# Optimization experiments

Measured on AMD Instinct MI355X. Metric: run time of the kernel, lower is better.

The kernel has to match this reference:

```python
import jax, jax.numpy as jnp
import numpy as np

B, IN, OUT = 8192, 4096, 2048  # OUT must equal 32*64 per betta/gamma sizes


def setup_inputs() -> dict:
    key = jax.random.key(0)
    kx, kw = jax.random.split(key, 2)
    X = jax.random.normal(kx, (B, IN), dtype=jnp.float32)
    # xavier-uniform-like init for W
    limit = float(np.sqrt(6.0 / (IN + OUT)))
    W = jax.random.uniform(kw, (IN, OUT), minval=-limit, maxval=limit, dtype=jnp.float32)
    absmean = jnp.abs(W).mean(axis=0)
    alpha = jnp.abs(W).mean()          # scalar, >= 0
    betta = absmean[:32]               # (32,), >= 0
    gamma = absmean[32:96]             # (64,), >= 0
    return {"X": X, "W": W, "alpha": alpha, "betta": betta, "gamma": gamma}


def reference(X, W, alpha, betta, gamma):
    # module applies relu_ to alpha/betta/gamma data before the functional call
    alpha = jax.nn.relu(alpha)
    betta = jax.nn.relu(betta)
    gamma = jax.nn.relu(gamma)
    X_bin = jnp.sign(X)                # (B, IN)
    W_bin = jnp.sign(W)                # (IN, OUT)
    # scale[i*64+j] = alpha * betta[i] * gamma[j] -> (OUT,)
    scale = (alpha * jnp.outer(betta, gamma)).reshape(-1)
    return (X_bin @ W_bin) * scale     # (B, OUT)
```

## Files before the change

### kernel.cpp

```cpp
#include <hip/hip_runtime.h>


#define M_DIM 8192
#define K_DIM 4096
#define N_DIM 2048
#define NTK   (K_DIM / 128)
#define PANEL (128 * 128 * 16)
#define KTILE 8192

typedef int i32x4 __attribute__((ext_vector_type(4)));
typedef int i32x8 __attribute__((ext_vector_type(8)));
typedef float f32x16 __attribute__((ext_vector_type(16)));

__device__ __forceinline__ unsigned int nib4(float x) {
  unsigned int s = (__float_as_uint(x) >> 28) & 0x8u;
  return x == 0.0f ? 0u : (0x2u | s);
}

__device__ __forceinline__ unsigned int pack8(const float* f) {
  unsigned int p = 0;
#pragma unroll
  for (int j = 0; j < 8; ++j) p |= nib4(f[j]) << (4 * j);
  return p;
}

__device__ __forceinline__ void gload_lds16(const void* g, void* lds) {
  __builtin_amdgcn_global_load_lds(
      (const __attribute__((address_space(1))) unsigned int*)g,
      (__attribute__((address_space(3))) unsigned int*)lds, 16, 0, 0);
}

__global__ __launch_bounds__(256) void binX_kernel(
    const float* __restrict__ X, unsigned char* __restrict__ Xq) {
  __shared__ float tile[32][260];
  const int t = threadIdx.x;
  const int rg = blockIdx.x >> 4;
  const int kc = blockIdx.x & 15;
  const int lrow = t >> 6;
  const int col4 = (t & 63) * 4;
#pragma unroll
  for (int i = 0; i < 8; ++i)
    *(float4*)&tile[i * 4 + lrow][col4] =
        *(const float4*)&X[(size_t)(rg * 32 + i * 4 + lrow) * K_DIM + kc * 256 + col4];
  __syncthreads();
  const int s = t >> 5;
  const int r = t & 31;
  float f[32];
#pragma unroll
  for (int q = 0; q < 8; ++q)
    *(float4*)&f[q * 4] = *(const float4*)&tile[r][s * 32 + q * 4];
  uint4 gq;
  gq.x = pack8(f + 0);  gq.y = pack8(f + 8);
  gq.z = pack8(f + 16); gq.w = pack8(f + 24);
  const int row = rg * 32 + r;
  const int kslot = kc * 8 + s;
  unsigned char* dst = Xq + (size_t)(row >> 7) * PANEL +
                       ((size_t)kslot * 128 + (row & 127)) * 16;
  *(uint4*)dst = gq;
}

__global__ __launch_bounds__(256) void binW_kernel(
    const float* __restrict__ W, unsigned char* __restrict__ Wq) {
  __shared__ float tile[32][260];
  const int t = threadIdx.x;
  const int q = blockIdx.x >> 7;
  const int kt = (blockIdx.x >> 3) & 15;
  const int s = blockIdx.x & 7;
#pragma unroll
  for (int i = 0; i < 8; ++i) {
    int row = i * 4 + (t >> 6);
    int col4 = (t & 63) * 4;
    *(float4*)&tile[row][col4] =
        *(const float4*)&W[(size_t)(kt * 256 + s * 32 + row) * N_DIM + q * 256 + col4];
  }
  __syncthreads();
  float f[32];
#pragma unroll
  for (int k = 0; k < 32; ++k) f[k] = tile[k][t];
  uint4 gq;
  gq.x = pack8(f + 0);  gq.y = pack8(f + 8);
  gq.z = pack8(f + 16); gq.w = pack8(f + 24);
  const int n = q * 256 + t;
  const int kslot = kt * 8 + s;
  unsigned char* dst = Wq + (size_t)(n >> 7) * PANEL +
                       ((size_t)kslot * 128 + (n & 127)) * 16;
  *(uint4*)dst = gq;
}

__device__ __forceinline__ void stage_tiles(const unsigned char* __restrict__ Asrc,
                                            const unsigned char* __restrict__ Bsrc,
                                            unsigned char* lds, int t) {
#pragma unroll
  for (int p = 0; p < 2; ++p) {
    int c = p * 256 + t;
    gload_lds16(Asrc + c * 16, lds + c * 16);
    gload_lds16(Bsrc + c * 16, lds + 8192 + c * 16);
  }
}

__global__ __launch_bounds__(256, 4) void gemm_fp4_kernel(
    const unsigned char* __restrict__ Aq,
    const unsigned char* __restrict__ Bq,
    const float* __restrict__ alpha,
    const float* __restrict__ betta,
    const float* __restrict__ gamma,
    float* __restrict__ C) {
  __shared__ __align__(16) unsigned char smem[32768];

  const int t = threadIdx.x;
  const int lane = t & 63;
  const int l31 = lane & 31;
  const int lhi = lane >> 5;
  const int w = t >> 6;
  const int wr = w >> 1;
  const int wc = w & 1;

  const int bid = blockIdx.x;
  const int j = bid >> 3;
  const int bn = j & 15;
  const int bm = (bid & 7) * 8 + (j >> 4);
  const int row0 = bm * 128;
  const int col0 = bn * 128;

  const unsigned char* Abase = Aq + (size_t)bm * PANEL;
  const unsigned char* Bbase = Bq + (size_t)bn * PANEL;

  f32x16 acc[2][2];
#pragma unroll
  for (int fm = 0; fm < 2; ++fm)
#pragma unroll
    for (int fn = 0; fn < 2; ++fn)
#pragma unroll
      for (int r = 0; r < 16; ++r) acc[fm][fn][r] = 0.f;

  i32x8 a8[2], b8[2];
#pragma unroll
  for (int i = 0; i < 2; ++i)
#pragma unroll
    for (int e = 0; e < 8; ++e) { a8[i][e] = 0; b8[i][e] = 0; }

  stage_tiles(Abase, Bbase, &smem[0], t);
  asm volatile("s_waitcnt vmcnt(0)" ::: "memory");
  __builtin_amdgcn_s_barrier();

  for (int kt = 0; kt < NTK; ++kt) {
    const int cur = kt & 1;
    const unsigned char* pA = &smem[cur * 16384];
    const unsigned char* pB = pA + 8192;

    if (kt + 1 < NTK)
      stage_tiles(Abase + (kt + 1) * KTILE, Bbase + (kt + 1) * KTILE,
                  &smem[(cur ^ 1) * 16384], t);

#pragma unroll
    for (int kk = 0; kk < 2; ++kk) {
      const int g = kk * 2 + lhi;
#pragma unroll
      for (int fm = 0; fm < 2; ++fm)
        *(i32x4*)&a8[fm] = *(const i32x4*)&pA[(g * 128 + wr * 64 + fm * 32 + l31) * 16];
#pragma unroll
      for (int fn = 0; fn < 2; ++fn)
        *(i32x4*)&b8[fn] = *(const i32x4*)&pB[(g * 128 + wc * 64 + fn * 32 + l31) * 16];
#pragma unroll
      for (int fm = 0; fm < 2; ++fm)
#pragma unroll
        for (int fn = 0; fn < 2; ++fn)
          acc[fm][fn] = __builtin_amdgcn_mfma_scale_f32_32x32x64_f8f6f4(
              a8[fm], b8[fn], acc[fm][fn], 4, 4,
              0, 0x7F7F7F7F, 0, 0x7F7F7F7F);
    }

    asm volatile("s_waitcnt vmcnt(0)" ::: "memory");
    __builtin_amdgcn_s_barrier();
  }

  const float ra = fmaxf(alpha[0], 0.0f);
#pragma unroll
  for (int fn = 0; fn < 2; ++fn) {
    const int col = col0 + wc * 64 + fn * 32 + l31;
    const float sc = ra * fmaxf(betta[col >> 6], 0.0f) * fmaxf(gamma[col & 63], 0.0f);
#pragma unroll
    for (int fm = 0; fm < 2; ++fm) {
      const int rbase = row0 + wr * 64 + fm * 32 + 4 * lhi;
#pragma unroll
      for (int r = 0; r < 16; ++r) {
        const int row = rbase + (r & 3) + 8 * (r >> 2);
        C[(size_t)row * N_DIM + col] = acc[fm][fn][r] * sc;
      }
    }
  }
}

extern "C" void kernel_launch(void* const* d_in, const int* in_sizes, int n_in,
                              void* d_out, int out_size, void* d_ws, size_t ws_size,
                              hipStream_t stream) {
  const float* X = (const float*)d_in[0];
  const float* W = (const float*)d_in[1];
  const float* alpha = (const float*)d_in[2];
  const float* betta = (const float*)d_in[3];
  const float* gamma = (const float*)d_in[4];
  float* out = (float*)d_out;

  unsigned char* Xq = (unsigned char*)d_ws;
  unsigned char* Wq = Xq + (size_t)(M_DIM / 128) * PANEL;

  binW_kernel<<<1024, 256, 0, stream>>>(W, Wq);
  binX_kernel<<<4096, 256, 0, stream>>>(X, Xq);
  gemm_fp4_kernel<<<(M_DIM / 128) * (N_DIM / 128), 256, 0, stream>>>(
      Xq, Wq, alpha, betta, gamma, out);
}
```

Before: 75.75 us.

## Enlarge GEMM tile to 256x128 with triple-buffered LDS pipeline

```diff
diff --git a/kernel.cpp b/kernel.cpp
--- a/kernel.cpp
+++ b/kernel.cpp
@@ -6,7 +6,8 @@
 #define N_DIM 2048
 #define NTK   (K_DIM / 128)
 #define PANEL (128 * 128 * 16)
-#define KTILE 8192
+#define KSTEP 8192
+#define BUFB  24576
 
 typedef int i32x4 __attribute__((ext_vector_type(4)));
 typedef int i32x8 __attribute__((ext_vector_type(8)));
@@ -87,25 +88,14 @@
   *(uint4*)dst = gq;
 }
 
-__device__ __forceinline__ void stage_tiles(const unsigned char* __restrict__ Asrc,
-                                            const unsigned char* __restrict__ Bsrc,
-                                            unsigned char* lds, int t) {
-#pragma unroll
-  for (int p = 0; p < 2; ++p) {
-    int c = p * 256 + t;
-    gload_lds16(Asrc + c * 16, lds + c * 16);
-    gload_lds16(Bsrc + c * 16, lds + 8192 + c * 16);
-  }
-}
-
-__global__ __launch_bounds__(256, 4) void gemm_fp4_kernel(
+__global__ __launch_bounds__(256, 2) void gemm_fp4_kernel(
     const unsigned char* __restrict__ Aq,
     const unsigned char* __restrict__ Bq,
     const float* __restrict__ alpha,
     const float* __restrict__ betta,
     const float* __restrict__ gamma,
     float* __restrict__ C) {
-  __shared__ __align__(16) unsigned char smem[32768];
+  __shared__ __align__(16) unsigned char smem[3 * BUFB];
 
   const int t = threadIdx.x;
   const int lane = t & 63;
@@ -117,62 +107,89 @@
 
   const int bid = blockIdx.x;
   const int j = bid >> 3;
-  const int bn = j & 15;
-  const int bm = (bid & 7) * 8 + (j >> 4);
-  const int row0 = bm * 128;
+  const int bm = (bid & 7) * 4 + (j & 3);
+  const int bn = j >> 2;
+  const int row0 = bm * 256;
   const int col0 = bn * 128;
 
-  const unsigned char* Abase = Aq + (size_t)bm * PANEL;
-  const unsigned char* Bbase = Bq + (size_t)bn * PANEL;
-
-  f32x16 acc[2][2];
-#pragma unroll
-  for (int fm = 0; fm < 2; ++fm)
+  const unsigned char* Asrc0 = Aq + (size_t)(2 * bm) * PANEL;
+  const unsigned char* Asrc1 = Asrc0 + PANEL;
+  const unsigned char* Bsrc  = Bq + (size_t)bn * PANEL;
+
+  f32x16 acc[4][2];
+#pragma unroll
+  for (int fm = 0; fm < 4; ++fm)
 #pragma unroll
     for (int fn = 0; fn < 2; ++fn)
 #pragma unroll
       for (int r = 0; r < 16; ++r) acc[fm][fn][r] = 0.f;
 
-  i32x8 a8[2], b8[2];
+  i32x8 a8[4], b8[2];
+#pragma unroll
+  for (int i = 0; i < 4; ++i)
+#pragma unroll
+    for (int e = 0; e < 8; ++e) a8[i][e] = 0;
 #pragma unroll
   for (int i = 0; i < 2; ++i)
 #pragma unroll
-    for (int e = 0; e < 8; ++e) { a8[i][e] = 0; b8[i][e] = 0; }
-
-  stage_tiles(Abase, Bbase, &smem[0], t);
-  asm volatile("s_waitcnt vmcnt(0)" ::: "memory");
-  __builtin_amdgcn_s_barrier();
-
-  for (int kt = 0; kt < NTK; ++kt) {
-    const int cur = kt & 1;
-    const unsigned char* pA = &smem[cur * 16384];
-    const unsigned char* pB = pA + 8192;
-
-    if (kt + 1 < NTK)
-      stage_tiles(Abase + (kt + 1) * KTILE, Bbase + (kt + 1) * KTILE,
-                  &smem[(cur ^ 1) * 16384], t);
-
+    for (int e = 0; e < 8; ++e) b8[i][e] = 0;
+
+  auto stage = [&](int kt, unsigned char* buf) {
+    const unsigned char* a0 = Asrc0 + kt * KSTEP;
+    const unsigned char* a1 = Asrc1 + kt * KSTEP;
+    const unsigned char* b  = Bsrc  + kt * KSTEP;
+#pragma unroll
+    for (int p = 0; p < 2; ++p) {
+      const int c = p * 256 + t;
+      gload_lds16(a0 + c * 16, buf + c * 16);
+      gload_lds16(a1 + c * 16, buf + 8192 + c * 16);
+      gload_lds16(b  + c * 16, buf + 16384 + c * 16);
+    }
+  };
+
+  auto compute = [&](const unsigned char* buf) {
+    const unsigned char* pA = buf + wr * 8192;
+    const unsigned char* pB = buf + 16384;
 #pragma unroll
     for (int kk = 0; kk < 2; ++kk) {
       const int g = kk * 2 + lhi;
 #pragma unroll
-      for (int fm = 0; fm < 2; ++fm)
-        *(i32x4*)&a8[fm] = *(const i32x4*)&pA[(g * 128 + wr * 64 + fm * 32 + l31) * 16];
+      for (int fm = 0; fm < 4; ++fm)
+        *(i32x4*)&a8[fm] = *(const i32x4*)&pA[(g * 128 + fm * 32 + l31) * 16];
 #pragma unroll
       for (int fn = 0; fn < 2; ++fn)
         *(i32x4*)&b8[fn] = *(const i32x4*)&pB[(g * 128 + wc * 64 + fn * 32 + l31) * 16];
-#pragma unroll
-      for (int fm = 0; fm < 2; ++fm)
+      __builtin_amdgcn_s_setprio(1);
+#pragma unroll
+      for (int fm = 0; fm < 4; ++fm)
 #pragma unroll
         for (int fn = 0; fn < 2; ++fn)
           acc[fm][fn] = __builtin_amdgcn_mfma_scale_f32_32x32x64_f8f6f4(
               a8[fm], b8[fn], acc[fm][fn], 4, 4,
               0, 0x7F7F7F7F, 0, 0x7F7F7F7F);
+      __builtin_amdgcn_s_setprio(0);
     }
-
-    asm volatile("s_waitcnt vmcnt(0)" ::: "memory");
+  };
+
+  unsigned char* P0 = smem;
+  unsigned char* P1 = smem + BUFB;
+  unsigned char* P2 = smem + 2 * BUFB;
+
+  stage(0, P0);
+  stage(1, P1);
+
+  for (int kt = 0; kt < NTK - 1; ++kt) {
+    asm volatile("s_waitcnt vmcnt(6)" ::: "memory");
     __builtin_amdgcn_s_barrier();
+    __builtin_amdgcn_sched_barrier(0);
+    if (kt + 2 < NTK) stage(kt + 2, P2);
+    compute(P0);
+    unsigned char* tmp = P0; P0 = P1; P1 = P2; P2 = tmp;
   }
+  asm volatile("s_waitcnt vmcnt(0)" ::: "memory");
+  __builtin_amdgcn_s_barrier();
+  __builtin_amdgcn_sched_barrier(0);
+  compute(P0);
 
   const float ra = fmaxf(alpha[0], 0.0f);
 #pragma unroll
@@ -180,8 +197,8 @@
     const int col = col0 + wc * 64 + fn * 32 + l31;
     const float sc = ra * fmaxf(betta[col >> 6], 0.0f) * fmaxf(gamma[col & 63], 0.0f);
 #pragma unroll
-    for (int fm = 0; fm < 2; ++fm) {
-      const int rbase = row0 + wr * 64 + fm * 32 + 4 * lhi;
+    for (int fm = 0; fm < 4; ++fm) {
+      const int rbase = row0 + wr * 128 + fm * 32 + 4 * lhi;
 #pragma unroll
       for (int r = 0; r < 16; ++r) {
         const int row = rbase + (r & 3) + 8 * (r >> 2);
@@ -206,6 +223,6 @@
 
   binW_kernel<<<1024, 256, 0, stream>>>(W, Wq);
   binX_kernel<<<4096, 256, 0, stream>>>(X, Xq);
-  gemm_fp4_kernel<<<(M_DIM / 128) * (N_DIM / 128), 256, 0, stream>>>(
+  gemm_fp4_kernel<<<(M_DIM / 256) * (N_DIM / 128), 256, 0, stream>>>(
       Xq, Wq, alpha, betta, gamma, out);
 }
```

After: 72.82 us. -3.9%, faster.
